# Performance work log

Hardware: AMD Instinct MI355X
Metric: run time of the kernel (lower is better)

Reference implementation:

```python
import jax, jax.numpy as jnp
import numpy as np

H = 1024

def _cell(xt, h, c, Wi, bi, Wh, bh):
    # gates: [B, 4H], torch Linear is x @ W.T + b; gate order i,f,g,o
    gates = xt @ Wi.T + bi + h @ Wh.T + bh
    i, f, g, o = jnp.split(gates, 4, axis=1)
    i = jax.nn.sigmoid(i)
    f = jax.nn.sigmoid(f)
    g = jnp.tanh(g)
    o = jax.nn.sigmoid(o)
    c_next = f * c + i * g
    h_next = o * jnp.tanh(c_next)
    return h_next, c_next

def setup_inputs() -> dict:
    key = jax.random.key(0)
    ks = jax.random.split(key, 12)
    vocab, E, out_dim = 32000, 1024, 32000
    B, T = 32, 512
    std = 1.0 / np.sqrt(H)
    u = lambda k, shape: jax.random.uniform(k, shape, jnp.float32, -std, std)
    return {
        "x": jax.random.randint(ks[0], (B, T), 0, vocab, dtype=jnp.int32),
        "emb": jax.random.normal(ks[1], (vocab, E), jnp.float32),
        "Wi0": u(ks[2], (4 * H, E)),  "bi0": u(ks[3], (4 * H,)),
        "Wh0": u(ks[4], (4 * H, H)), "bh0": u(ks[5], (4 * H,)),
        "Wi1": u(ks[6], (4 * H, H)), "bi1": u(ks[7], (4 * H,)),
        "Wh1": u(ks[8], (4 * H, H)), "bh1": u(ks[9], (4 * H,)),
        "fc_w": u(ks[10], (out_dim, H)) * (std * np.sqrt(H)) / np.sqrt(H),
        "fc_b": u(ks[11], (out_dim,)),
    }

def reference(x, emb, Wi0, bi0, Wh0, bh0, Wi1, bi1, Wh1, bh1, fc_w, fc_b):
    B, T = x.shape
    xe = emb[x]  # [B, T, E]
    xe = jnp.transpose(xe, (1, 0, 2))  # [T, B, E]
    init = (jnp.zeros((B, H), xe.dtype), jnp.zeros((B, H), xe.dtype),
            jnp.zeros((B, H), xe.dtype), jnp.zeros((B, H), xe.dtype))

    def step(carry, xt):
        h0, c0, h1, c1 = carry
        h0, c0 = _cell(xt, h0, c0, Wi0, bi0, Wh0, bh0)
        h1, c1 = _cell(h0, h1, c1, Wi1, bi1, Wh1, bh1)
        return (h0, c0, h1, c1), None

    (h0, c0, h1, c1), _ = jax.lax.scan(step, init, xe)
    return h1 @ fc_w.T + fc_b  # [B, out_dim]
```

## Files before the change

kernel.cpp:

```cpp
#include <hip/hip_runtime.h>
#include <hip/hip_bf16.h>

typedef __attribute__((ext_vector_type(8))) short short8;
typedef __attribute__((ext_vector_type(4))) float f32x4;
typedef __attribute__((ext_vector_type(4))) int i32x4;
typedef unsigned short u16;
typedef unsigned int u32;
typedef unsigned long long u64;

#define MFMA_BF16(a, b, c) __builtin_amdgcn_mfma_f32_16x16x32_bf16((a), (b), (c), 0, 0, 0)

static constexpr size_t OFF_W   = 0;
static constexpr size_t OFF_B0  = 33554432;
static constexpr size_t OFF_B1  = OFF_B0 + 16384;
static constexpr size_t OFF_H0  = OFF_B1 + 16384;
static constexpr size_t OFF_H1F = OFF_H0 + 262144;
static constexpr size_t OFF_XE  = OFF_H1F + 131072;
static constexpr size_t OFF_X0  = OFF_XE + 33554432;
static constexpr size_t WS_NEED = OFF_X0 + 134217728;
static constexpr size_t OFF_FLG = OFF_X0 - 4096;


__device__ __forceinline__ u16 f2bf(float f) {
  u32 x = __builtin_bit_cast(u32, f);
  x += 0x7fffu + ((x >> 16) & 1u);
  return (u16)(x >> 16);
}
__device__ __forceinline__ float bf2f(u16 u) {
  return __builtin_bit_cast(float, (u32)u << 16);
}
__device__ __forceinline__ float sigm(float x) { return 1.f / (1.f + expf(-x)); }

__device__ __forceinline__ void sysstore64(void* p, u64 v) {
  __hip_atomic_store((u64*)p, v, __ATOMIC_RELAXED, __HIP_MEMORY_SCOPE_SYSTEM);
}
__device__ __forceinline__ u64 sysload64(const void* p) {
  return __hip_atomic_load((const u64*)p, __ATOMIC_RELAXED, __HIP_MEMORY_SCOPE_SYSTEM);
}

__device__ __forceinline__ void gload_lds16(const u16* gsrc, u16* ldst) {
  __builtin_amdgcn_global_load_lds(
      (__attribute__((address_space(1))) void*)(u16*)gsrc,
      (__attribute__((address_space(3))) void*)ldst, 16, 0, 0);
}

__global__ void prep_w_kernel(const float* __restrict__ Wi0, const float* __restrict__ Wh0,
                              const float* __restrict__ Wi1, const float* __restrict__ Wh1,
                              u16* __restrict__ dst) {
  size_t e = ((size_t)blockIdx.x * 256 + threadIdx.x) * 4;
  int mat = (int)(e >> 22);
  size_t off = e & ((1ull << 22) - 1);
  const float* src = (mat == 0) ? Wi0 : (mat == 1) ? Wh0 : (mat == 2) ? Wi1 : Wh1;
  float4 v = *(const float4*)(src + off);
  ushort4 o;
  o.x = f2bf(v.x); o.y = f2bf(v.y); o.z = f2bf(v.z); o.w = f2bf(v.w);
  *(ushort4*)(dst + e) = o;
}

__global__ void prep_b_kernel(const float* __restrict__ bi0, const float* __restrict__ bh0,
                              const float* __restrict__ bi1, const float* __restrict__ bh1,
                              float* __restrict__ b0, float* __restrict__ b1) {
  int i = blockIdx.x * 256 + threadIdx.x;
  b0[i] = bi0[i] + bh0[i];
  b1[i] = bi1[i] + bh1[i];
}

__global__ void embed_kernel(const int* __restrict__ x, const float* __restrict__ emb,
                             u16* __restrict__ xe) {
  int m = blockIdx.x;
  int b = m & 31, t = m >> 5;
  int id = x[b * 512 + t];
  float4 v = ((const float4*)(emb + (size_t)id * 1024))[threadIdx.x];
  ushort4 o;
  o.x = f2bf(v.x); o.y = f2bf(v.y); o.z = f2bf(v.z); o.w = f2bf(v.w);
  *(ushort4*)(xe + (size_t)m * 1024 + threadIdx.x * 4) = o;
}

__global__ void x0_gemm_kernel(const u16* __restrict__ A, const u16* __restrict__ W,
                               const float* __restrict__ bias, u16* __restrict__ Xp) {
  __shared__ u16 lds[2][2][8192];
  const int tid = threadIdx.x, l = tid & 63, w = tid >> 6;
  const int n0 = blockIdx.x * 128, m0 = blockIdx.y * 128;
  const int wm = w >> 1, wn = w & 1;
  const int row8 = l >> 3, u = l & 7;

  f32x4 acc[4][4];
#pragma unroll
  for (int a1 = 0; a1 < 4; ++a1)
#pragma unroll
    for (int a2 = 0; a2 < 4; ++a2) acc[a1][a2] = (f32x4){0.f, 0.f, 0.f, 0.f};

  auto stage = [&](int buf, int kt) {
    const int k0 = kt * 64;
#pragma unroll
    for (int q = 0; q < 4; ++q) {
      const int ld = w * 4 + q;
      const int row = ld * 8 + row8;
      const int sw = (u ^ (row & 7)) * 8;
      gload_lds16(A + (size_t)(m0 + row) * 1024 + k0 + sw, &lds[buf][0][ld * 512]);
      gload_lds16(W + (size_t)(n0 + row) * 1024 + k0 + sw, &lds[buf][1][ld * 512]);
    }
  };

  stage(0, 0);
  __syncthreads();

  for (int kt = 0; kt < 16; ++kt) {
    const int buf = kt & 1;
    if (kt < 15) stage(buf ^ 1, kt + 1);
    const u16* la = lds[buf][0];
    const u16* lb = lds[buf][1];
#pragma unroll
    for (int kk = 0; kk < 2; ++kk) {
      const int c = kk * 4 + (l >> 4);
      const int csw = (c ^ (l & 7)) * 8;
      short8 af[4], bf[4];
#pragma unroll
      for (int mi = 0; mi < 4; ++mi) {
        int row = wm * 64 + mi * 16 + (l & 15);
        af[mi] = *(const short8*)(la + row * 64 + csw);
      }
#pragma unroll
      for (int ni = 0; ni < 4; ++ni) {
        int row = wn * 64 + ni * 16 + (l & 15);
        bf[ni] = *(const short8*)(lb + row * 64 + csw);
      }
#pragma unroll
      for (int mi = 0; mi < 4; ++mi)
#pragma unroll
        for (int ni = 0; ni < 4; ++ni)
          acc[mi][ni] = MFMA_BF16(af[mi], bf[ni], acc[mi][ni]);
    }
    __syncthreads();
  }

#pragma unroll
  for (int ni = 0; ni < 4; ++ni) {
    int col = n0 + wn * 64 + ni * 16 + (l & 15);
    int g = col >> 10, blkid = (col & 1023) >> 2, j = col & 3;
    float bv = bias[col];
#pragma unroll
    for (int mi = 0; mi < 4; ++mi) {
#pragma unroll
      for (int r = 0; r < 4; ++r) {
        int row = m0 + wm * 64 + mi * 16 + (l >> 4) * 4 + r;
        int t = row >> 5, b = row & 31;
        Xp[(size_t)t * 131072 + blkid * 512 + b * 16 + j * 4 + g] =
            f2bf(acc[mi][ni][r] + bv);
      }
    }
  }
}

__launch_bounds__(256, 1)
__global__ void lstm_kernel(const u16* __restrict__ wbf, const float* __restrict__ b1v,
                            const u16* __restrict__ Xp, u16* __restrict__ hinit,
                            float* __restrict__ h1f, u32* __restrict__ flagsD) {
  extern __shared__ char smem[];
  u16* wlds = (u16*)smem;
  float* gates0 = (float*)(smem + 98304);
  float* part1  = (float*)(smem + 98304 + 2048);
  float* wh1p   = (float*)(smem + 98304 + 4096);

  const int tid = threadIdx.x;
  const int l = tid & 63, w = tid >> 6;
  const int blk = blockIdx.x;
  const int hbase = blk * 4;
  u16* Xw = (u16*)Xp;

  for (int m = 0; m < 3; ++m) {
    const u16* Wm = wbf + (size_t)(m + 1) * (4096 * 1024);
    for (int s = tid; s < 2048; s += 256) {
      int kk = s >> 6, ll = s & 63;
      int nl = ll & 15, hi = ll >> 4;
      int gr = (nl >> 2) * 1024 + hbase + (nl & 3);
      short8 v = *(const short8*)(Wm + (size_t)gr * 1024 + kk * 32 + hi * 8);
      *(short8*)(wlds + m * 16384 + kk * 512 + ll * 8) = v;
    }
  }
  __syncthreads();

  float cst = 0.f;
  const int at = tid & 127, ab = at >> 2, aj = at & 3;
  const int mt = w & 1;

  float b1i = 0.f, b1fv = 0.f, b1g = 0.f, b1o = 0.f;
  if (tid >= 128) {
    b1i  = b1v[hbase + aj];
    b1fv = b1v[1024 + hbase + aj];
    b1g  = b1v[2048 + hbase + aj];
    b1o  = b1v[3072 + hbase + aj];
  }

  u64 gchunk = 0;
  if (tid < 128)
    gchunk = sysload64(Xp + blk * 512 + ab * 16 + aj * 4);

  const u32* fquad = flagsD + l * 4;

  for (int i = 0; i <= 512; ++i) {
    const u16* slot_r = (i == 0) ? hinit
                      : (i == 1) ? hinit + 65536
                                 : Xp + (size_t)(i - 2) * 131072;
    u16* slot_w = (i == 0) ? hinit + 65536
                           : Xw + (size_t)(i - 1) * 131072;

    asm volatile("" ::: "memory");

    const u16* abase = slot_r + (w < 2 ? 0 : 32768)
                     + (mt * 16 + (l & 15)) * 1024 + ((l >> 4) * 8);
    short8 ar[32];
#pragma unroll
    for (int kk = 0; kk < 32; ++kk)
      ar[kk] = *(const short8*)(abase + kk * 32);

    if (w < 2) {
      f32x4 a0a = {0,0,0,0}, a0b = {0,0,0,0}, a1a = {0,0,0,0}, a1b = {0,0,0,0};
#pragma unroll
      for (int kk = 0; kk < 16; ++kk) {
        a0a = MFMA_BF16(ar[2 * kk],     *(const short8*)(wlds + (2 * kk) * 512 + l * 8), a0a);
        a1a = MFMA_BF16(ar[2 * kk],     *(const short8*)(wlds + 16384 + (2 * kk) * 512 + l * 8), a1a);
        a0b = MFMA_BF16(ar[2 * kk + 1], *(const short8*)(wlds + (2 * kk + 1) * 512 + l * 8), a0b);
        a1b = MFMA_BF16(ar[2 * kk + 1], *(const short8*)(wlds + 16384 + (2 * kk + 1) * 512 + l * 8), a1b);
      }
#pragma unroll
      for (int r = 0; r < 4; ++r) {
        int row = mt * 16 + (l >> 4) * 4 + r, col = l & 15;
        gates0[row * 16 + col] = a0a[r] + a0b[r];
        part1[row * 16 + col]  = a1a[r] + a1b[r];
      }
    } else {
      f32x4 a0a = {0,0,0,0}, a0b = {0,0,0,0};
#pragma unroll
      for (int kk = 0; kk < 16; ++kk) {
        a0a = MFMA_BF16(ar[2 * kk],     *(const short8*)(wlds + 2 * 16384 + (2 * kk) * 512 + l * 8), a0a);
        a0b = MFMA_BF16(ar[2 * kk + 1], *(const short8*)(wlds + 2 * 16384 + (2 * kk + 1) * 512 + l * 8), a0b);
      }
#pragma unroll
      for (int r = 0; r < 4; ++r) {
        int row = mt * 16 + (l >> 4) * 4 + r, col = l & 15;
        wh1p[row * 16 + col] = a0a[r] + a0b[r];
      }
    }
    __syncthreads();

    if (tid < 128) {
      if (i < 512) {
        float gi = gates0[ab * 16 + aj]      + bf2f((u16)(gchunk));
        float gf = gates0[ab * 16 + 4 + aj]  + bf2f((u16)(gchunk >> 16));
        float gg = gates0[ab * 16 + 8 + aj]  + bf2f((u16)(gchunk >> 32));
        float go = gates0[ab * 16 + 12 + aj] + bf2f((u16)(gchunk >> 48));
        cst = sigm(gf) * cst + sigm(gi) * tanhf(gg);
        float h = sigm(go) * tanhf(cst);
        u32 hv = (u32)f2bf(h);
        u32 p1 = (u32)__shfl_xor((int)hv, 1);
        u32 lo = (aj & 1) ? ((p1 & 0xffff) | (hv << 16)) : ((hv & 0xffff) | (p1 << 16));
        u32 p2 = (u32)__shfl_xor((int)lo, 2);
        if (aj == 0)
          sysstore64(slot_w + ab * 1024 + hbase, (u64)lo | ((u64)p2 << 32));
      }
    } else {
      if (i >= 1) {
        float gi = part1[ab * 16 + aj]      + wh1p[ab * 16 + aj]      + b1i;
        float gf = part1[ab * 16 + 4 + aj]  + wh1p[ab * 16 + 4 + aj]  + b1fv;
        float gg = part1[ab * 16 + 8 + aj]  + wh1p[ab * 16 + 8 + aj]  + b1g;
        float go = part1[ab * 16 + 12 + aj] + wh1p[ab * 16 + 12 + aj] + b1o;
        cst = sigm(gf) * cst + sigm(gi) * tanhf(gg);
        float h = sigm(go) * tanhf(cst);
        u32 hv = (u32)f2bf(h);
        u32 p1 = (u32)__shfl_xor((int)hv, 1);
        u32 lo = (aj & 1) ? ((p1 & 0xffff) | (hv << 16)) : ((hv & 0xffff) | (p1 << 16));
        u32 p2 = (u32)__shfl_xor((int)lo, 2);
        if (aj == 0)
          sysstore64(slot_w + 32768 + ab * 1024 + hbase, (u64)lo | ((u64)p2 << 32));
        if (i == 512) h1f[ab * 1024 + hbase + aj] = h;
      }
    }

    if (i == 512) break;

    __syncthreads();
    const u32 target = (u32)(i + 1);
    if (tid == 0)
      __hip_atomic_store(&flagsD[blk], target, __ATOMIC_RELAXED, __HIP_MEMORY_SCOPE_SYSTEM);

    if (tid < 128 && i + 1 < 512)
      gchunk = sysload64(Xp + (size_t)(i + 1) * 131072 + blk * 512 + ab * 16 + aj * 4);

    if (w == 0) {
      while (true) {
        i32x4 v;
        asm volatile("global_load_dwordx4 %0, %1, off sc0 sc1"
                     : "=&v"(v) : "v"(fquad));
        asm volatile("s_waitcnt vmcnt(0)" ::: "memory");
        u32 m01 = min((u32)v.x, (u32)v.y);
        u32 m23 = min((u32)v.z, (u32)v.w);
        if (__all(min(m01, m23) >= target)) break;
      }
    }
    __syncthreads();
  }
}

__global__ void fc_kernel(const float* __restrict__ h1f, const float* __restrict__ fcw,
                          const float* __restrict__ fcb, float* __restrict__ out) {
  int gid = blockIdx.x * 256 + threadIdx.x;
  int v = gid >> 5, b = gid & 31;
  const float4* wr = (const float4*)(fcw + (size_t)v * 1024);
  const float4* hr = (const float4*)(h1f + (size_t)b * 1024);
  float s = 0.f;
#pragma unroll 8
  for (int i = 0; i < 256; ++i) {
    float4 wv = wr[i], hv = hr[i];
    s += wv.x * hv.x + wv.y * hv.y + wv.z * hv.z + wv.w * hv.w;
  }
  out[(size_t)b * 32000 + v] = s + fcb[v];
}

extern "C" void kernel_launch(void* const* d_in, const int* in_sizes, int n_in,
                              void* d_out, int out_size, void* d_ws, size_t ws_size,
                              hipStream_t stream) {
  const int*   x   = (const int*)d_in[0];
  const float* emb = (const float*)d_in[1];
  const float* Wi0 = (const float*)d_in[2];
  const float* bi0 = (const float*)d_in[3];
  const float* Wh0 = (const float*)d_in[4];
  const float* bh0 = (const float*)d_in[5];
  const float* Wi1 = (const float*)d_in[6];
  const float* bi1 = (const float*)d_in[7];
  const float* Wh1 = (const float*)d_in[8];
  const float* bh1 = (const float*)d_in[9];
  const float* fcw = (const float*)d_in[10];
  const float* fcb = (const float*)d_in[11];
  float* out = (float*)d_out;
  char* ws = (char*)d_ws;

  if (ws_size < WS_NEED) return;

  u16*   wbf = (u16*)(ws + OFF_W);
  float* b0v = (float*)(ws + OFF_B0);
  float* b1v = (float*)(ws + OFF_B1);
  u16*   hin = (u16*)(ws + OFF_H0);
  float* h1f = (float*)(ws + OFF_H1F);
  u16*   xe  = (u16*)(ws + OFF_XE);
  u16*   Xp  = (u16*)(ws + OFF_X0);
  u32*   flg = (u32*)(ws + OFF_FLG);

  hipMemsetAsync(ws + OFF_H0, 0, OFF_XE - OFF_H0, stream);

  prep_w_kernel<<<16384, 256, 0, stream>>>(Wi0, Wh0, Wi1, Wh1, wbf);
  prep_b_kernel<<<16, 256, 0, stream>>>(bi0, bh0, bi1, bh1, b0v, b1v);
  embed_kernel<<<16384, 256, 0, stream>>>(x, emb, xe);
  x0_gemm_kernel<<<dim3(32, 128), 256, 0, stream>>>(xe, wbf, b0v, Xp);

  hipMemsetAsync(ws + OFF_FLG, 0, 4096, stream);

  hipFuncSetAttribute((const void*)lstm_kernel,
                      hipFuncAttributeMaxDynamicSharedMemorySize, 104448);
  lstm_kernel<<<256, 256, 104448, stream>>>(wbf, b1v, Xp, hin, h1f, flg);

  fc_kernel<<<4000, 256, 0, stream>>>(h1f, fcw, fcb, out);
}
```

Measured before the change: 3.805 ms.

## Split grid barrier into per-layer flags so layer-1 work overlaps layer-0 sync

The single per-step global flag array becomes two: flagsA, published right after the layer-0 hidden state is written, and flagsB, published after layer 1. The layer-0 cell update and its flag store now happen before the Wi1·h0 matmul and the layer-1 update. Other blocks can therefore start the next layer-0 step sooner, taking layer-1 work off the critical inter-block dependency chain. In exchange there is an extra __syncthreads, a second polling wave, and more intra-block serialization, since waves 0-1 now run their MFMAs in two phases.

```diff
diff --git a/kernel.cpp b/kernel.cpp
--- a/kernel.cpp
+++ b/kernel.cpp
@@ -42,6 +42,18 @@
   __builtin_amdgcn_global_load_lds(
       (__attribute__((address_space(1))) void*)(u16*)gsrc,
       (__attribute__((address_space(3))) void*)ldst, 16, 0, 0);
+}
+
+__device__ __forceinline__ void poll256(const u32* fquad, u32 target) {
+  while (true) {
+    i32x4 v;
+    asm volatile("global_load_dwordx4 %0, %1, off sc0 sc1"
+                 : "=&v"(v) : "v"(fquad));
+    asm volatile("s_waitcnt vmcnt(0)" ::: "memory");
+    u32 m01 = min((u32)v.x, (u32)v.y);
+    u32 m23 = min((u32)v.z, (u32)v.w);
+    if (__all(min(m01, m23) >= target)) break;
+  }
 }
 
 __global__ void prep_w_kernel(const float* __restrict__ Wi0, const float* __restrict__ Wh0,
@@ -155,7 +167,7 @@
 __launch_bounds__(256, 1)
 __global__ void lstm_kernel(const u16* __restrict__ wbf, const float* __restrict__ b1v,
                             const u16* __restrict__ Xp, u16* __restrict__ hinit,
-                            float* __restrict__ h1f, u32* __restrict__ flagsD) {
+                            float* __restrict__ h1f, u32* __restrict__ flagsA) {
   extern __shared__ char smem[];
   u16* wlds = (u16*)smem;
   float* gates0 = (float*)(smem + 98304);
@@ -166,6 +178,7 @@
   const int l = tid & 63, w = tid >> 6;
   const int blk = blockIdx.x;
   const int hbase = blk * 4;
+  u32* flagsB = flagsA + 256;
   u16* Xw = (u16*)Xp;
 
   for (int m = 0; m < 3; ++m) {
@@ -196,109 +209,114 @@
   if (tid < 128)
     gchunk = sysload64(Xp + blk * 512 + ab * 16 + aj * 4);
 
-  const u32* fquad = flagsD + l * 4;
+  const u32* fqA = flagsA + l * 4;
+  const u32* fqB = flagsB + l * 4;
 
   for (int i = 0; i <= 512; ++i) {
-    const u16* slot_r = (i == 0) ? hinit
-                      : (i == 1) ? hinit + 65536
-                                 : Xp + (size_t)(i - 2) * 131072;
-    u16* slot_w = (i == 0) ? hinit + 65536
-                           : Xw + (size_t)(i - 1) * 131072;
-
+    const u16* rh0 = (i == 0) ? hinit
+                   : (i == 1) ? hinit + 65536
+                              : Xp + (size_t)(i - 2) * 131072;
+    const u16* rh1 = (i <= 1) ? hinit + 32768
+                              : Xp + (size_t)(i - 2) * 131072 + 32768;
+    u16* wh0 = (i == 0) ? hinit + 65536 : Xw + (size_t)(i - 1) * 131072;
+    u16* wh1 = Xw + (size_t)(i - 1) * 131072 + 32768;
+
+    if (i) {
+      if (w == 0) poll256(fqA, (u32)i);
+      if (w == 2) poll256(fqB, (u32)i);
+    }
+    __syncthreads();
     asm volatile("" ::: "memory");
 
-    const u16* abase = slot_r + (w < 2 ? 0 : 32768)
-                     + (mt * 16 + (l & 15)) * 1024 + ((l >> 4) * 8);
+    const u16* abase = (w < 2 ? rh0 : rh1) + (mt * 16 + (l & 15)) * 1024 + ((l >> 4) * 8);
     short8 ar[32];
 #pragma unroll
     for (int kk = 0; kk < 32; ++kk)
       ar[kk] = *(const short8*)(abase + kk * 32);
 
     if (w < 2) {
-      f32x4 a0a = {0,0,0,0}, a0b = {0,0,0,0}, a1a = {0,0,0,0}, a1b = {0,0,0,0};
+      if (i < 512) {
+        f32x4 a0 = {0,0,0,0}, a1 = {0,0,0,0};
+#pragma unroll
+        for (int kk = 0; kk < 16; ++kk) {
+          a0 = MFMA_BF16(ar[2 * kk],     *(const short8*)(wlds + (2 * kk) * 512 + l * 8), a0);
+          a1 = MFMA_BF16(ar[2 * kk + 1], *(const short8*)(wlds + (2 * kk + 1) * 512 + l * 8), a1);
+        }
+#pragma unroll
+        for (int r = 0; r < 4; ++r) {
+          int row = mt * 16 + (l >> 4) * 4 + r, col = l & 15;
+          gates0[row * 16 + col] = a0[r] + a1[r];
+        }
+      }
+    } else {
+      f32x4 a0 = {0,0,0,0}, a1 = {0,0,0,0};
 #pragma unroll
       for (int kk = 0; kk < 16; ++kk) {
-        a0a = MFMA_BF16(ar[2 * kk],     *(const short8*)(wlds + (2 * kk) * 512 + l * 8), a0a);
-        a1a = MFMA_BF16(ar[2 * kk],     *(const short8*)(wlds + 16384 + (2 * kk) * 512 + l * 8), a1a);
-        a0b = MFMA_BF16(ar[2 * kk + 1], *(const short8*)(wlds + (2 * kk + 1) * 512 + l * 8), a0b);
-        a1b = MFMA_BF16(ar[2 * kk + 1], *(const short8*)(wlds + 16384 + (2 * kk + 1) * 512 + l * 8), a1b);
+        a0 = MFMA_BF16(ar[2 * kk],     *(const short8*)(wlds + 2 * 16384 + (2 * kk) * 512 + l * 8), a0);
+        a1 = MFMA_BF16(ar[2 * kk + 1], *(const short8*)(wlds + 2 * 16384 + (2 * kk + 1) * 512 + l * 8), a1);
       }
 #pragma unroll
       for (int r = 0; r < 4; ++r) {
         int row = mt * 16 + (l >> 4) * 4 + r, col = l & 15;
-        gates0[row * 16 + col] = a0a[r] + a0b[r];
-        part1[row * 16 + col]  = a1a[r] + a1b[r];
-      }
-    } else {
-      f32x4 a0a = {0,0,0,0}, a0b = {0,0,0,0};
+        wh1p[row * 16 + col] = a0[r] + a1[r];
+      }
+    }
+
+    if (tid < 128 && i < 512) {
+      float gi = gates0[ab * 16 + aj]      + bf2f((u16)(gchunk));
+      float gf = gates0[ab * 16 + 4 + aj]  + bf2f((u16)(gchunk >> 16));
+      float gg = gates0[ab * 16 + 8 + aj]  + bf2f((u16)(gchunk >> 32));
+      float go = gates0[ab * 16 + 12 + aj] + bf2f((u16)(gchunk >> 48));
+      cst = sigm(gf) * cst + sigm(gi) * tanhf(gg);
+      float h = sigm(go) * tanhf(cst);
+      u32 hv = (u32)f2bf(h);
+      u32 p1 = (u32)__shfl_xor((int)hv, 1);
+      u32 lo = (aj & 1) ? ((p1 & 0xffff) | (hv << 16)) : ((hv & 0xffff) | (p1 << 16));
+      u32 p2 = (u32)__shfl_xor((int)lo, 2);
+      if (aj == 0)
+        sysstore64(wh0 + ab * 1024 + hbase, (u64)lo | ((u64)p2 << 32));
+    }
+    __syncthreads();
+    if (tid == 0 && i < 512)
+      __hip_atomic_store(&flagsA[blk], (u32)(i + 1), __ATOMIC_RELAXED, __HIP_MEMORY_SCOPE_SYSTEM);
+
+    if (w < 2 && i >= 1) {
+      f32x4 a0 = {0,0,0,0}, a1 = {0,0,0,0};
 #pragma unroll
       for (int kk = 0; kk < 16; ++kk) {
-        a0a = MFMA_BF16(ar[2 * kk],     *(const short8*)(wlds + 2 * 16384 + (2 * kk) * 512 + l * 8), a0a);
-        a0b = MFMA_BF16(ar[2 * kk + 1], *(const short8*)(wlds + 2 * 16384 + (2 * kk + 1) * 512 + l * 8), a0b);
+        a0 = MFMA_BF16(ar[2 * kk],     *(const short8*)(wlds + 16384 + (2 * kk) * 512 + l * 8), a0);
+        a1 = MFMA_BF16(ar[2 * kk + 1], *(const short8*)(wlds + 16384 + (2 * kk + 1) * 512 + l * 8), a1);
       }
 #pragma unroll
       for (int r = 0; r < 4; ++r) {
         int row = mt * 16 + (l >> 4) * 4 + r, col = l & 15;
-        wh1p[row * 16 + col] = a0a[r] + a0b[r];
-      }
-    }
-    __syncthreads();
-
-    if (tid < 128) {
-      if (i < 512) {
-        float gi = gates0[ab * 16 + aj]      + bf2f((u16)(gchunk));
-        float gf = gates0[ab * 16 + 4 + aj]  + bf2f((u16)(gchunk >> 16));
-        float gg = gates0[ab * 16 + 8 + aj]  + bf2f((u16)(gchunk >> 32));
-        float go = gates0[ab * 16 + 12 + aj] + bf2f((u16)(gchunk >> 48));
-        cst = sigm(gf) * cst + sigm(gi) * tanhf(gg);
-        float h = sigm(go) * tanhf(cst);
-        u32 hv = (u32)f2bf(h);
-        u32 p1 = (u32)__shfl_xor((int)hv, 1);
-        u32 lo = (aj & 1) ? ((p1 & 0xffff) | (hv << 16)) : ((hv & 0xffff) | (p1 << 16));
-        u32 p2 = (u32)__shfl_xor((int)lo, 2);
-        if (aj == 0)
-          sysstore64(slot_w + ab * 1024 + hbase, (u64)lo | ((u64)p2 << 32));
-      }
-    } else {
-      if (i >= 1) {
-        float gi = part1[ab * 16 + aj]      + wh1p[ab * 16 + aj]      + b1i;
-        float gf = part1[ab * 16 + 4 + aj]  + wh1p[ab * 16 + 4 + aj]  + b1fv;
-        float gg = part1[ab * 16 + 8 + aj]  + wh1p[ab * 16 + 8 + aj]  + b1g;
-        float go = part1[ab * 16 + 12 + aj] + wh1p[ab * 16 + 12 + aj] + b1o;
-        cst = sigm(gf) * cst + sigm(gi) * tanhf(gg);
-        float h = sigm(go) * tanhf(cst);
-        u32 hv = (u32)f2bf(h);
-        u32 p1 = (u32)__shfl_xor((int)hv, 1);
-        u32 lo = (aj & 1) ? ((p1 & 0xffff) | (hv << 16)) : ((hv & 0xffff) | (p1 << 16));
-        u32 p2 = (u32)__shfl_xor((int)lo, 2);
-        if (aj == 0)
-          sysstore64(slot_w + 32768 + ab * 1024 + hbase, (u64)lo | ((u64)p2 << 32));
-        if (i == 512) h1f[ab * 1024 + hbase + aj] = h;
-      }
-    }
-
-    if (i == 512) break;
-
-    __syncthreads();
-    const u32 target = (u32)(i + 1);
-    if (tid == 0)
-      __hip_atomic_store(&flagsD[blk], target, __ATOMIC_RELAXED, __HIP_MEMORY_SCOPE_SYSTEM);
-
+        part1[row * 16 + col] = a0[r] + a1[r];
+      }
+    }
     if (tid < 128 && i + 1 < 512)
       gchunk = sysload64(Xp + (size_t)(i + 1) * 131072 + blk * 512 + ab * 16 + aj * 4);
-
-    if (w == 0) {
-      while (true) {
-        i32x4 v;
-        asm volatile("global_load_dwordx4 %0, %1, off sc0 sc1"
-                     : "=&v"(v) : "v"(fquad));
-        asm volatile("s_waitcnt vmcnt(0)" ::: "memory");
-        u32 m01 = min((u32)v.x, (u32)v.y);
-        u32 m23 = min((u32)v.z, (u32)v.w);
-        if (__all(min(m01, m23) >= target)) break;
-      }
-    }
-    __syncthreads();
+    __syncthreads();
+
+    if (tid >= 128 && i >= 1) {
+      float gi = part1[ab * 16 + aj]      + wh1p[ab * 16 + aj]      + b1i;
+      float gf = part1[ab * 16 + 4 + aj]  + wh1p[ab * 16 + 4 + aj]  + b1fv;
+      float gg = part1[ab * 16 + 8 + aj]  + wh1p[ab * 16 + 8 + aj]  + b1g;
+      float go = part1[ab * 16 + 12 + aj] + wh1p[ab * 16 + 12 + aj] + b1o;
+      cst = sigm(gf) * cst + sigm(gi) * tanhf(gg);
+      float h = sigm(go) * tanhf(cst);
+      u32 hv = (u32)f2bf(h);
+      u32 p1 = (u32)__shfl_xor((int)hv, 1);
+      u32 lo = (aj & 1) ? ((p1 & 0xffff) | (hv << 16)) : ((hv & 0xffff) | (p1 << 16));
+      u32 p2 = (u32)__shfl_xor((int)lo, 2);
+      if (aj == 0)
+        sysstore64(wh1 + ab * 1024 + hbase, (u64)lo | ((u64)p2 << 32));
+      if (i == 512) h1f[ab * 1024 + hbase + aj] = h;
+    }
+    if (i == 512) break;
+
+    __syncthreads();
+    if (tid == 0)
+      __hip_atomic_store(&flagsB[blk], (u32)(i + 1), __ATOMIC_RELAXED, __HIP_MEMORY_SCOPE_SYSTEM);
   }
 }
 
```

Measured after the change: 4.659 ms. +22.5%, slower.
